# Kernel tuning notes

Hardware: AMD Instinct MI355X
Metric: run time of the kernel (lower is better)

The kernel has to match this reference:

```python
import jax, jax.numpy as jnp
import numpy as np

EMB, GCN = 256, 256
N_REL = 200
B, E, TOPK = 256, 100000, 64
N_PREV, N_ENT, N_TIME = 50000, 20000, 2000


def _linear(x, w, b):
    # torch nn.Linear convention: w is [out, in]
    return x @ w.T + b


def setup_inputs() -> dict:
    key = jax.random.key(0)
    ks = jax.random.split(key, 32)
    nrm = lambda k, s: (jax.random.normal(k, s, jnp.float32) * 0.05)
    # facts columns: b, n, h, r, t, ts. b built so every batch has >= TOPK facts.
    b_col = jax.random.permutation(ks[0], jnp.arange(E, dtype=jnp.int32) % B)
    n_col = jax.random.randint(ks[1], (E,), 0, N_PREV, jnp.int32)
    h_col = jax.random.randint(ks[2], (E,), 0, N_ENT, jnp.int32)
    r_col = jax.random.randint(ks[3], (E,), 0, N_REL, jnp.int32)  # r+1 indexes [zero;rel]
    t_col = jax.random.randint(ks[4], (E,), 0, N_ENT, jnp.int32)
    ts_col = jax.random.randint(ks[5], (E,), 0, N_TIME, jnp.int32)
    facts = jnp.stack([b_col, n_col, h_col, r_col, t_col, ts_col], axis=1)
    return {
        "query_time": jax.random.randint(ks[6], (B,), 0, N_TIME, jnp.int32),  # unused by forward
        "query_emd": nrm(ks[7], (B, EMB)),
        "temp_neighbors_facts": facts,
        "ent_emd": nrm(ks[8], (N_ENT, GCN)),
        "rel_emd": nrm(ks[9], (N_REL, GCN)),
        "hidden_node": nrm(ks[10], (N_PREV, EMB)),
        "hidden_rel": nrm(ks[11], (N_PREV, EMB)),
        "hidden_time": nrm(ks[12], (N_PREV, EMB)),  # unused by forward
        "att_agg": jax.random.uniform(ks[13], (N_PREV,), jnp.float32),
        "time_emd": nrm(ks[14], (N_TIME, EMB)),
        "zero_rel_emd": nrm(ks[15], (1, GCN)),
        "W_message_w": nrm(ks[16], (EMB, 2 * EMB)), "W_message_b": jnp.zeros((EMB,), jnp.float32),
        "att_1_w": nrm(ks[17], (1, 3 * EMB)), "att_1_b": jnp.zeros((1,), jnp.float32),
        "att_2_w": nrm(ks[18], (1, EMB)), "att_2_b": jnp.zeros((1,), jnp.float32),
        "W_h_w": nrm(ks[19], (EMB, 2 * EMB)), "W_h_b": jnp.zeros((EMB,), jnp.float32),
        "lin_e_ts_w": nrm(ks[20], (EMB, GCN + EMB)), "lin_e_ts_b": jnp.zeros((EMB,), jnp.float32),
        "lin_r_ts_w": nrm(ks[21], (EMB, GCN)), "lin_r_ts_b": jnp.zeros((EMB,), jnp.float32),
        "lin_time_w": nrm(ks[22], (EMB, EMB)), "lin_time_b": jnp.zeros((EMB,), jnp.float32),
        "gru_w_ih": nrm(ks[23], (3 * EMB, EMB)), "gru_w_hh": nrm(ks[24], (3 * EMB, EMB)),
        "gru_b_ih": jnp.zeros((3 * EMB,), jnp.float32), "gru_b_hh": jnp.zeros((3 * EMB,), jnp.float32),
        "batch_size": B, "device": 0, "max_nodes": TOPK,
    }


def reference(query_time, query_emd, temp_neighbors_facts, ent_emd, rel_emd,
              hidden_node, hidden_rel, hidden_time, att_agg, time_emd,
              zero_rel_emd, W_message_w, W_message_b, att_1_w, att_1_b,
              att_2_w, att_2_b, W_h_w, W_h_b, lin_e_ts_w, lin_e_ts_b,
              lin_r_ts_w, lin_r_ts_b, lin_time_w, lin_time_b,
              gru_w_ih, gru_w_hh, gru_b_ih, gru_b_hh,
              batch_size, device, max_nodes):
    f = temp_neighbors_facts
    b, n, r, t, ts = f[:, 0], f[:, 1], f[:, 3], f[:, 4], f[:, 5]

    hidden_node_pre = hidden_node[n]            # [E, EMB]
    hidden_rel_pre = hidden_rel[n]              # [E, EMB]
    rel_all = jnp.concatenate([zero_rel_emd, rel_emd], axis=0)
    h_r = rel_all[r + 1]                        # [E, GCN]
    h_ts_raw = time_emd[ts]                     # [E, EMB]
    h_t = _linear(jnp.concatenate([ent_emd[t], h_ts_raw], -1), lin_e_ts_w, lin_e_ts_b)
    h_r = _linear(h_r, lin_r_ts_w, lin_r_ts_b)
    _ = _linear(h_ts_raw, lin_time_w, lin_time_b)  # computed but unused in original

    message = _linear(jnp.concatenate([hidden_node_pre, h_r], -1), W_message_w, W_message_b)
    att_input = jnp.concatenate([query_emd[b], message, h_t], -1)  # [E, 3*EMB]
    att1 = jax.nn.sigmoid(_linear(att_input, att_1_w, att_1_b))[:, 0]

    # single-step GRU (torch nn.GRU gate math)
    gi = h_r @ gru_w_ih.T + gru_b_ih            # [E, 3*EMB]
    gh = hidden_rel_pre @ gru_w_hh.T + gru_b_hh
    i_r, i_z, i_n = jnp.split(gi, 3, axis=-1)
    h_rg, h_zg, h_ng = jnp.split(gh, 3, axis=-1)
    rg = jax.nn.sigmoid(i_r + h_rg)
    zg = jax.nn.sigmoid(i_z + h_zg)
    ng = jnp.tanh(i_n + rg * h_ng)
    hidden_rel_new = (1.0 - zg) * ng + zg * hidden_rel_pre

    att2 = jax.nn.sigmoid(_linear(hidden_rel_new, att_2_w, att_2_b))[:, 0]
    attention = (att1 + att2) * 0.5

    # vectorized per-batch top-k (each batch is guaranteed >= max_nodes facts)
    order = jnp.lexsort((-attention, b))        # sort by batch asc, attention desc
    counts = jax.ops.segment_sum(jnp.ones_like(b), b, num_segments=batch_size)
    starts = jnp.cumsum(counts) - counts
    sel = (starts[:, None] + jnp.arange(max_nodes)[None, :]).reshape(-1)
    new_index = order[sel]                      # [B*topk]

    facts_k = f[new_index]
    message = message[new_index]
    hidden_rel_new = hidden_rel_new[new_index]
    attention = (att1[new_index] + att2[new_index]) * 0.5
    b_k, n_k = facts_k[:, 0], facts_k[:, 1]
    attention = attention * att_agg[n_k]
    M = b_k.shape[0]

    rows = facts_k[:, jnp.array([0, 4, 5])]     # (b, t, ts)
    tail_nodes, tail_index = jnp.unique(rows, axis=0, size=M, fill_value=0, return_inverse=True)
    tail_index = tail_index.reshape(-1)

    tail_emd = _linear(jnp.concatenate([ent_emd[tail_nodes[:, 1]], time_emd[tail_nodes[:, 2]]], -1),
                       lin_e_ts_w, lin_e_ts_b)

    # group_max_norm: normalize attention by per-batch sum (0/0 -> 0)
    den = jax.ops.segment_sum(attention, b_k, num_segments=batch_size)[b_k]
    safe_den = jnp.where(den != 0, den, 1.0)
    attention = jnp.where(den != 0, attention / safe_den, 0.0)

    message_agg = jax.ops.segment_sum(attention[:, None] * message, tail_index, num_segments=M)
    hidden_node_new = _linear(jnp.concatenate([message_agg, tail_emd], -1), W_h_w, W_h_b)  # act = identity
    hidden_rel_out = jax.ops.segment_sum(attention[:, None] * hidden_rel_new, tail_index, num_segments=M)
    att_agg_new = jax.ops.segment_sum(attention, tail_index, num_segments=M)
    return tail_nodes, hidden_node_new, hidden_rel_out, att_agg_new
```

## Files before the change

### kernel.cpp

```cpp
#include <hip/hip_runtime.h>
#include <hip/hip_bf16.h>

#define E_N    100000
#define B_N    256
#define TOPK   64
#define NPREV  50000
#define NENT   20000
#define NTIME  2000
#define NREL   200
#define M_OUT  16384
#define NT8    6250

static __device__ __forceinline__ float sigm(float x){ return 1.f/(1.f+expf(-x)); }

__global__ void zero_kernel(unsigned* __restrict__ p, int n){
  int i = blockIdx.x*256 + threadIdx.x;
  if (i < n) p[i] = 0u;
}

__global__ void pack_w_kernel(const float* __restrict__ w_msg,
                              const float* __restrict__ w_hh,
                              const float* __restrict__ lets_w,
                              const float* __restrict__ w_h,
                              float4* __restrict__ wP,
                              float4* __restrict__ wPL,
                              float4* __restrict__ wPH){
  int i = blockIdx.x*256 + threadIdx.x;
  if (i < 65536){
    int t = i & 255, mat = (i >> 8) & 3, kblk = i >> 10;
    float4 v;
    if (mat == 0) v = *(const float4*)&w_msg[(size_t)t*512 + kblk*4];
    else          v = *(const float4*)&w_hh[(size_t)((mat-1)*256 + t)*256 + kblk*4];
    wP[i] = v;
  } else if (i < 98304){
    int j = i - 65536;
    int t = j & 255, mat = (j >> 8) & 1, kblk = j >> 9;
    wPL[j] = *(const float4*)&lets_w[(size_t)t*512 + mat*256 + kblk*4];
  } else if (i < 131072){
    int j = i - 98304;
    int t = j & 255, kblk = j >> 8;
    wPH[j] = *(const float4*)&w_h[(size_t)t*512 + kblk*4];
  }
}

__global__ void matvec_fused(const float* __restrict__ w_msg,
                             const float* __restrict__ lets_w,
                             const float* __restrict__ lets_b,
                             const float* __restrict__ att1w,
                             const float* __restrict__ att1b,
                             float* __restrict__ wm1a, float* __restrict__ ve,
                             float* __restrict__ vts, float* __restrict__ consts){
  int blk = blockIdx.x, t = threadIdx.x;
  if (blk == 3){
    if (t < 64){
      float p = 0.f;
      for (int d = t; d < 256; d += 64) p += lets_b[d]*att1w[512+d];
      for (int o = 32; o > 0; o >>= 1) p += __shfl_down(p, o);
      if (t == 0) consts[0] = att1b[0] + p;
    }
    return;
  }
  const float* M; int moff; const float* v; float* out;
  if (blk == 0){ M = w_msg;  moff = 0;   v = att1w+256; out = wm1a; }
  else if (blk == 1){ M = lets_w; moff = 0;   v = att1w+512; out = ve; }
  else { M = lets_w; moff = 256; v = att1w+512; out = vts; }
  float acc = 0.f;
  for (int d = 0; d < 256; ++d) acc += M[(size_t)d*512 + moff + t] * v[d];
  out[t] = acc;
}

__global__ void rows_dot_multi(
    const float* __restrict__ A0, const float* __restrict__ v0, float* __restrict__ o0, int n0,
    const float* __restrict__ A1, const float* __restrict__ v1, float* __restrict__ o1_, int n1,
    const float* __restrict__ A2, const float* __restrict__ v2, float* __restrict__ o2, int n2,
    const float* __restrict__ A3, const float* __restrict__ v3, float* __restrict__ o3, int n3,
    const float* __restrict__ A4, const float* __restrict__ v4, float* __restrict__ o4, int n4){
  int gid = blockIdx.x*256 + threadIdx.x;
  int wid = gid >> 6, lane = gid & 63;
  const float* A; const float* v; float* o; int r;
  if (wid < n0){ A=A0; v=v0; o=o0; r=wid; }
  else if ((wid -= n0) < n1){ A=A1; v=v1; o=o1_; r=wid; }
  else if ((wid -= n1) < n2){ A=A2; v=v2; o=o2; r=wid; }
  else if ((wid -= n2) < n3){ A=A3; v=v3; o=o3; r=wid; }
  else if ((wid -= n3) < n4){ A=A4; v=v4; o=o4; r=wid; }
  else return;
  const float* row = A + (size_t)r*256;
  float p = 0.f;
  for (int k = lane; k < 256; k += 64) p += row[k]*v[k];
  for (int off = 32; off > 0; off >>= 1) p += __shfl_down(p, off);
  if (lane == 0) o[r] = p;
}

template<int ND>
__global__ __launch_bounds__(256) void tile_linear(
    const float* __restrict__ A, int lda,
    const float* __restrict__ Bw, int ldb, int boff,
    const float* __restrict__ bias,
    float* __restrict__ out, int ldo, int rows){
  __shared__ float a_s[16][260];
  int tile0 = blockIdx.x*16;
  for (int idx = threadIdx.x; idx < 16*256; idx += 256){
    int i = idx >> 8, k = idx & 255;
    int row = tile0 + i;
    a_s[i][k] = (row < rows) ? A[(size_t)row*lda + k] : 0.f;
  }
  __syncthreads();
  int d = threadIdx.x;
  const float* brow[ND];
  #pragma unroll
  for (int q = 0; q < ND; ++q) brow[q] = Bw + (size_t)(d + 256*q)*ldb + boff;
  float acc[ND][16];
  #pragma unroll
  for (int q = 0; q < ND; ++q){
    float bv = bias ? bias[d + 256*q] : 0.f;
    #pragma unroll
    for (int i = 0; i < 16; ++i) acc[q][i] = bv;
  }
  for (int k = 0; k < 256; k += 4){
    float4 w[ND];
    #pragma unroll
    for (int q = 0; q < ND; ++q) w[q] = *(const float4*)(brow[q] + k);
    #pragma unroll
    for (int i = 0; i < 16; ++i){
      float4 a = *(const float4*)&a_s[i][k];
      #pragma unroll
      for (int q = 0; q < ND; ++q)
        acc[q][i] += w[q].x*a.x + w[q].y*a.y + w[q].z*a.z + w[q].w*a.w;
    }
  }
  #pragma unroll
  for (int i = 0; i < 16; ++i){
    int row = tile0 + i;
    if (row < rows){
      #pragma unroll
      for (int q = 0; q < ND; ++q) out[(size_t)row*ldo + d + 256*q] = acc[q][i];
    }
  }
}

__global__ __launch_bounds__(256) void gemv_ets(
    const float* __restrict__ act, const float4* __restrict__ wPL, int matsel,
    const float* __restrict__ bias, float* __restrict__ out){
  int tile0 = blockIdx.x*16, t = threadIdx.x;
  float acc[16];
  float bv = bias ? bias[t] : 0.f;
  #pragma unroll
  for (int p = 0; p < 16; ++p) acc[p] = bv;
  float4 w = wPL[matsel*256 + t];
  for (int kb = 0; kb < 64; ++kb){
    int kbn = (kb + 1) & 63;
    float4 nw = wPL[(kbn*2 + matsel)*256 + t];
    int k = kb*4;
    #pragma unroll
    for (int p = 0; p < 16; ++p){
      float4 a = *(const float4*)&act[(size_t)(tile0+p)*256 + k];
      acc[p] += w.x*a.x + w.y*a.y + w.z*a.z + w.w*a.w;
    }
    w = nw;
  }
  #pragma unroll
  for (int p = 0; p < 16; ++p)
    out[(size_t)(tile0+p)*256 + t] = acc[p];
}

__global__ void hist2_kernel(const int* __restrict__ facts,
                             int* __restrict__ cnt_t, int* __restrict__ cnt_b){
  int e = blockIdx.x*256 + threadIdx.x;
  if (e < E_N){
    atomicAdd(&cnt_t[facts[e*6+1] >> 3], 1);
    atomicAdd(&cnt_b[facts[e*6+0]], 1);
  }
}

__global__ void scan2_kernel(const int* __restrict__ cnt_t, int* __restrict__ off_t, int* __restrict__ cur_t,
                             const int* __restrict__ cnt_b, int* __restrict__ off_b, int* __restrict__ cur_b){
  const int* cnt; int* off; int* cur; int n;
  if (blockIdx.x == 0){ cnt = cnt_t; off = off_t; cur = cur_t; n = NT8; }
  else { cnt = cnt_b; off = off_b; cur = cur_b; n = B_N; }
  int lane = threadIdx.x;
  int run = 0;
  int npad = (n + 63) & ~63;
  for (int base = 0; base < npad; base += 64){
    int idx = base + lane;
    int orig = (idx < n) ? cnt[idx] : 0;
    int v = orig;
    for (int o = 1; o < 64; o <<= 1){ int t = __shfl_up(v, o); if (lane >= o) v += t; }
    if (idx < n){ int ex = run + v - orig; off[idx] = ex; cur[idx] = ex; }
    run += __shfl(v, 63);
  }
  if (lane == 0) off[n] = E_N;
}

__global__ void scatter2_kernel(const int* __restrict__ facts,
                                int* __restrict__ cur_t, int* __restrict__ edges_t,
                                int* __restrict__ cur_b, int* __restrict__ edges_b){
  int e = blockIdx.x*256 + threadIdx.x;
  if (e < E_N){
    int pt = atomicAdd(&cur_t[facts[e*6+1] >> 3], 1);
    edges_t[pt] = e;
    int pb = atomicAdd(&cur_b[facts[e*6+0]], 1);
    edges_b[pb] = e;
  }
}

__global__ __launch_bounds__(256) void att_kernel(
    const float* __restrict__ hidden_rel,
    const float4* __restrict__ wP,
    const float* __restrict__ b_hh,
    const float* __restrict__ gi,
    const float* __restrict__ att2w, const float* __restrict__ att2b,
    const int* __restrict__ facts,
    const int* __restrict__ bin_off, const int* __restrict__ bin_edges,
    const float* __restrict__ qdot, const float* __restrict__ sn_m,
    const float* __restrict__ sr_m, const float* __restrict__ se,
    const float* __restrict__ st,   const float* __restrict__ consts,
    float* __restrict__ attention){
  __shared__ float gh_s[8][776];
  int tile0 = blockIdx.x*8;
  int t = threadIdx.x;

  float acc[3][8];
  #pragma unroll
  for (int q = 0; q < 3; ++q)
    #pragma unroll
    for (int p = 0; p < 8; ++p) acc[q][p] = 0.f;

  float4 w1 = wP[256 + t], w2 = wP[512 + t], w3 = wP[768 + t];
  for (int kb = 0; kb < 64; ++kb){
    int kbn = (kb + 1) & 63;
    int nb = (kbn*4)*256 + t;
    float4 nw1 = wP[nb + 256], nw2 = wP[nb + 512], nw3 = wP[nb + 768];
    int k = kb*4;
    #pragma unroll
    for (int p = 0; p < 8; ++p){
      float4 a = *(const float4*)&hidden_rel[(size_t)(tile0+p)*256 + k];
      acc[0][p] += w1.x*a.x + w1.y*a.y + w1.z*a.z + w1.w*a.w;
      acc[1][p] += w2.x*a.x + w2.y*a.y + w2.z*a.z + w2.w*a.w;
      acc[2][p] += w3.x*a.x + w3.y*a.y + w3.z*a.z + w3.w*a.w;
    }
    w1 = nw1; w2 = nw2; w3 = nw3;
  }
  #pragma unroll
  for (int q = 0; q < 3; ++q){
    float bv = b_hh[t + 256*q];
    #pragma unroll
    for (int p = 0; p < 8; ++p)
      gh_s[p][t + 256*q] = acc[q][p] + bv;
  }
  __syncthreads();

  int wv = t >> 6, l = t & 63;
  int o0 = bin_off[blockIdx.x], o1 = bin_off[blockIdx.x + 1];
  int d0 = 4*l;
  float4 a2 = *(const float4*)&att2w[d0];
  float c1 = consts[0];
  float a2b = att2b[0];
  for (int idx = o0 + wv; idx < o1; idx += 4){
    int e  = bin_edges[idx];
    int b  = facts[e*6+0], n = facts[e*6+1], r = facts[e*6+3];
    int t_ = facts[e*6+4], ts_ = facts[e*6+5];
    int nl = n - tile0;
    float4 ghr = *(const float4*)&gh_s[nl][d0];
    float4 ghz = *(const float4*)&gh_s[nl][256+d0];
    float4 ghn = *(const float4*)&gh_s[nl][512+d0];
    const float* girow = gi + (size_t)r*768;
    float4 gir = *(const float4*)&girow[d0];
    float4 giz = *(const float4*)&girow[256+d0];
    float4 gin = *(const float4*)&girow[512+d0];
    float4 hp  = *(const float4*)&hidden_rel[(size_t)n*256 + d0];
    float partial;
    {
      float rg = sigm(gir.x + ghr.x), zg = sigm(giz.x + ghz.x);
      float ng = tanhf(gin.x + rg*ghn.x);
      partial = a2.x * ((1.f - zg)*ng + zg*hp.x);
    }{
      float rg = sigm(gir.y + ghr.y), zg = sigm(giz.y + ghz.y);
      float ng = tanhf(gin.y + rg*ghn.y);
      partial += a2.y * ((1.f - zg)*ng + zg*hp.y);
    }{
      float rg = sigm(gir.z + ghr.z), zg = sigm(giz.z + ghz.z);
      float ng = tanhf(gin.z + rg*ghn.z);
      partial += a2.z * ((1.f - zg)*ng + zg*hp.z);
    }{
      float rg = sigm(gir.w + ghr.w), zg = sigm(giz.w + ghz.w);
      float ng = tanhf(gin.w + rg*ghn.w);
      partial += a2.w * ((1.f - zg)*ng + zg*hp.w);
    }
    #pragma unroll
    for (int o = 32; o > 0; o >>= 1) partial += __shfl_xor(partial, o);
    if (l == 0){
      float att2 = sigm(partial + a2b);
      float x1 = qdot[b] + sn_m[n] + sr_m[r] + se[t_] + st[ts_] + c1;
      attention[e] = 0.5f*(sigm(x1) + att2);
    }
  }
}

__global__ __launch_bounds__(256) void topk_kernel(
    const int* __restrict__ facts, const float* __restrict__ attention,
    const float* __restrict__ att_agg,
    const int* __restrict__ boff, const int* __restrict__ bedges,
    int* __restrict__ sel_edge, float* __restrict__ att_norm,
    unsigned* __restrict__ skey, int* __restrict__ Ub){
  __shared__ float sa[512];
  __shared__ int   si[512];
  __shared__ unsigned sk[64];
  int b = blockIdx.x, tid = threadIdx.x;
  sa[tid] = -1.f; sa[tid+256] = -1.f;
  si[tid] = 0x7fffffff; si[tid+256] = 0x7fffffff;
  __syncthreads();
  int o0 = boff[b], cnt = boff[b+1] - o0;
  for (int i = tid; i < cnt; i += 256){
    int e = bedges[o0 + i];
    sa[i] = attention[e]; si[i] = e;
  }
  __syncthreads();
  for (int k = 2; k <= 512; k <<= 1){
    for (int j = k >> 1; j > 0; j >>= 1){
      for (int i0 = tid; i0 < 512; i0 += 256){
        int l = i0 ^ j;
        if (l > i0){
          float ai = sa[i0], al = sa[l];
          int   ii = si[i0], il = si[l];
          bool lFirst = (al > ai) || (al == ai && il < ii);
          bool up = ((i0 & k) == 0);
          if (up ? lFirst : !lFirst){
            sa[i0] = al; sa[l] = ai; si[i0] = il; si[l] = ii;
          }
        }
      }
      __syncthreads();
    }
  }
  if (tid < 64){
    int e = si[tid];
    bool valid = (e != 0x7fffffff);
    if (!valid) e = 0;
    int n = facts[e*6+1];
    float a = valid ? sa[tid]*att_agg[n] : 0.f;
    float den = a;
    for (int o = 32; o > 0; o >>= 1) den += __shfl_down(den, o);
    den = __shfl(den, 0);
    float norm = (den != 0.f) ? a/den : 0.f;
    sel_edge[b*64 + tid] = e;
    att_norm[b*64 + tid] = norm;
    int t_ = facts[e*6+4], ts_ = facts[e*6+5];
    unsigned key = (((unsigned)t_) << 11) | (unsigned)ts_;
    sk[tid] = (key << 6) | (unsigned)tid;
  }
  __syncthreads();
  for (int k = 2; k <= 64; k <<= 1){
    for (int j = k >> 1; j > 0; j >>= 1){
      unsigned nv = 0; bool act = tid < 64;
      if (act){
        unsigned mine = sk[tid], other = sk[tid ^ j];
        bool up = ((tid & k) == 0);
        bool keepmin = (up == ((tid & j) == 0));
        nv = keepmin ? (mine < other ? mine : other) : (mine > other ? mine : other);
      }
      __syncthreads();
      if (act) sk[tid] = nv;
      __syncthreads();
    }
  }
  if (tid < 64){
    unsigned kk = sk[tid];
    skey[b*64 + tid] = kk;
    bool head = (tid == 0) || ((kk >> 6) != (sk[tid-1] >> 6));
    unsigned long long bal = __ballot(head);
    if (tid == 0) Ub[b] = __popcll(bal);
  }
}

__global__ void offs_scan_kernel(const int* __restrict__ Ub, int* __restrict__ offs){
  int lane = threadIdx.x;
  int run = 0;
  for (int base = 0; base < 256; base += 64){
    int orig = Ub[base + lane];
    int v = orig;
    for (int o = 1; o < 64; o <<= 1){ int t = __shfl_up(v, o); if (lane >= o) v += t; }
    offs[base + lane] = run + v - orig;
    run += __shfl(v, 63);
  }
  if (lane == 0) offs[256] = run;
}

__global__ void emit_kernel(const unsigned* __restrict__ skey, const int* __restrict__ offs,
                            int* __restrict__ us, int* __restrict__ tails,
                            float* __restrict__ out_tail){
  int b = blockIdx.x, tid = threadIdx.x;
  unsigned kk = skey[b*64 + tid];
  bool head = (tid == 0) || ((kk >> 6) != (skey[b*64 + tid - 1] >> 6));
  unsigned long long bal = __ballot(head);
  unsigned long long mask_le = (tid == 63) ? ~0ull : ((1ull << (tid+1)) - 1ull);
  int ulocal = __popcll(bal & mask_le) - 1;
  int u = offs[b] + ulocal;
  us[b*64 + tid] = u;
  if (head){
    unsigned key = kk >> 6;
    int t_ = (int)(key >> 11), ts_ = (int)(key & 2047u);
    tails[u*3+0] = b; tails[u*3+1] = t_; tails[u*3+2] = ts_;
    out_tail[u*3+0] = (float)b;
    out_tail[u*3+1] = (float)t_;
    out_tail[u*3+2] = (float)ts_;
  }
}

__global__ __launch_bounds__(256) void sel_kernel(
    const unsigned* __restrict__ skey, const int* __restrict__ sel_edge,
    const float* __restrict__ att_norm, const int* __restrict__ facts,
    const float* __restrict__ hidden_node, const float* __restrict__ hidden_rel,
    const float4* __restrict__ wP,
    const float* __restrict__ msg_r, const float* __restrict__ gi,
    const float* __restrict__ b_hh,
    float* __restrict__ msg_sel, float* __restrict__ hrn_sel){
  __shared__ int n_s[8], r_s[8];
  __shared__ float av_s[8];
  int base = blockIdx.x*8;
  int t = threadIdx.x;
  if (t < 8){
    int gs = base + t;
    int b = gs >> 6, i = gs & 63;
    int j = (int)(skey[(size_t)b*64 + i] & 63u);
    int s = b*64 + j;
    int e = sel_edge[s];
    n_s[t] = facts[e*6+1];
    r_s[t] = facts[e*6+3];
    av_s[t] = att_norm[s];
  }
  __syncthreads();

  float acc[4][8];
  #pragma unroll
  for (int q = 0; q < 4; ++q)
    #pragma unroll
    for (int e = 0; e < 8; ++e) acc[q][e] = 0.f;

  float4 w0 = wP[t], w1 = wP[256 + t], w2 = wP[512 + t], w3 = wP[768 + t];
  for (int kb = 0; kb < 64; ++kb){
    int kbn = (kb + 1) & 63;
    int nb = (kbn*4)*256 + t;
    float4 nw0 = wP[nb], nw1 = wP[nb + 256], nw2 = wP[nb + 512], nw3 = wP[nb + 768];
    int k = kb*4;
    #pragma unroll
    for (int e = 0; e < 8; ++e){
      float4 an = *(const float4*)&hidden_node[(size_t)n_s[e]*256 + k];
      float4 ah = *(const float4*)&hidden_rel[(size_t)n_s[e]*256 + k];
      acc[0][e] += w0.x*an.x + w0.y*an.y + w0.z*an.z + w0.w*an.w;
      acc[1][e] += w1.x*ah.x + w1.y*ah.y + w1.z*ah.z + w1.w*ah.w;
      acc[2][e] += w2.x*ah.x + w2.y*ah.y + w2.z*ah.z + w2.w*ah.w;
      acc[3][e] += w3.x*ah.x + w3.y*ah.y + w3.z*ah.z + w3.w*ah.w;
    }
    w0 = nw0; w1 = nw1; w2 = nw2; w3 = nw3;
  }

  float bhr = b_hh[t], bhz = b_hh[256+t], bhn = b_hh[512+t];
  #pragma unroll
  for (int e = 0; e < 8; ++e){
    int r = r_s[e]; float a = av_s[e];
    const float* girow = gi + (size_t)r*768;
    float msgv = acc[0][e] + msg_r[(size_t)r*256 + t];
    float rg = sigm(girow[t]      + acc[1][e] + bhr);
    float zg = sigm(girow[256+t]  + acc[2][e] + bhz);
    float ng = tanhf(girow[512+t] + rg*(acc[3][e] + bhn));
    float hp = hidden_rel[(size_t)n_s[e]*256 + t];
    float hrn = (1.f - zg)*ng + zg*hp;
    size_t o = (size_t)(base + e)*256 + t;
    msg_sel[o] = a*msgv;
    hrn_sel[o] = a*hrn;
  }
}

__global__ __launch_bounds__(256) void segsum_kernel(
    const unsigned* __restrict__ skey, const int* __restrict__ us,
    const float* __restrict__ att_norm,
    const float* __restrict__ msg_sel, const float* __restrict__ hrn_sel,
    float* __restrict__ msg_agg, float* __restrict__ out_hrel,
    float* __restrict__ out_aagg){
  int b = blockIdx.x, d = threadIdx.x;
  float accm = 0.f, acch = 0.f, acca = 0.f;
  int ucur = -1;
  for (int i = 0; i < 64; ++i){
    int u = us[b*64 + i];
    if (u != ucur){
      if (ucur >= 0){
        msg_agg[(size_t)ucur*256 + d] = accm;
        out_hrel[(size_t)ucur*256 + d] = acch;
        if (d == 0) out_aagg[ucur] = acca;
      }
      ucur = u; accm = 0.f; acch = 0.f; acca = 0.f;
    }
    size_t o = (size_t)(b*64 + i)*256 + d;
    accm += msg_sel[o];
    acch += hrn_sel[o];
    int j = (int)(skey[b*64 + i] & 63u);
    acca += att_norm[b*64 + j];
  }
  if (ucur >= 0){
    msg_agg[(size_t)ucur*256 + d] = accm;
    out_hrel[(size_t)ucur*256 + d] = acch;
    if (d == 0) out_aagg[ucur] = acca;
  }
}

__global__ __launch_bounds__(256) void final_kernel(
    const float* __restrict__ msg_agg, const int* __restrict__ tails,
    const float* __restrict__ ent_t, const float* __restrict__ time_t,
    const float4* __restrict__ wPH,
    const float* __restrict__ b_h,
    float* __restrict__ out_hn){
  int tile0 = blockIdx.x*16, t = threadIdx.x;
  int tu[16], tsu[16];
  #pragma unroll
  for (int p = 0; p < 16; ++p){
    tu[p]  = tails[(tile0+p)*3+1];
    tsu[p] = tails[(tile0+p)*3+2];
  }
  float acc[16];
  float bv = b_h[t];
  #pragma unroll
  for (int p = 0; p < 16; ++p) acc[p] = bv;
  float4 w = wPH[t];
  for (int kb = 0; kb < 128; ++kb){
    int kbn = (kb + 1) & 127;
    float4 nw = wPH[kbn*256 + t];
    if (kb < 64){
      int k = kb*4;
      #pragma unroll
      for (int p = 0; p < 16; ++p){
        float4 a = *(const float4*)&msg_agg[(size_t)(tile0+p)*256 + k];
        acc[p] += w.x*a.x + w.y*a.y + w.z*a.z + w.w*a.w;
      }
    } else {
      int k = (kb-64)*4;
      #pragma unroll
      for (int p = 0; p < 16; ++p){
        float4 a1 = *(const float4*)&ent_t[(size_t)tu[p]*256 + k];
        float4 a2 = *(const float4*)&time_t[(size_t)tsu[p]*256 + k];
        float ax = a1.x + a2.x, ay = a1.y + a2.y, az = a1.z + a2.z, aw = a1.w + a2.w;
        acc[p] += w.x*ax + w.y*ay + w.z*az + w.w*aw;
      }
    }
    w = nw;
  }
  #pragma unroll
  for (int p = 0; p < 16; ++p)
    out_hn[(size_t)(tile0+p)*256 + t] = acc[p];
}

extern "C" void kernel_launch(void* const* d_in, const int* in_sizes, int n_in,
                              void* d_out, int out_size, void* d_ws, size_t ws_size,
                              hipStream_t stream){
  const float* query_emd   = (const float*)d_in[1];
  const int*   facts       = (const int*)  d_in[2];
  const float* ent_emd     = (const float*)d_in[3];
  const float* rel_emd     = (const float*)d_in[4];
  const float* hidden_node = (const float*)d_in[5];
  const float* hidden_rel  = (const float*)d_in[6];
  const float* att_agg     = (const float*)d_in[8];
  const float* time_emd    = (const float*)d_in[9];
  const float* w_msg       = (const float*)d_in[11];
  const float* b_msg       = (const float*)d_in[12];
  const float* att1w       = (const float*)d_in[13];
  const float* att1b       = (const float*)d_in[14];
  const float* att2w       = (const float*)d_in[15];
  const float* att2b       = (const float*)d_in[16];
  const float* w_h         = (const float*)d_in[17];
  const float* b_h         = (const float*)d_in[18];
  const float* lets_w      = (const float*)d_in[19];
  const float* lets_b      = (const float*)d_in[20];
  const float* lrts_w      = (const float*)d_in[21];
  const float* lrts_b      = (const float*)d_in[22];
  const float* w_ih        = (const float*)d_in[25];
  const float* w_hh        = (const float*)d_in[26];
  const float* b_ih        = (const float*)d_in[27];
  const float* b_hh        = (const float*)d_in[28];

  char* p = (char*)d_ws;
  auto alloc = [&](size_t bytes) -> void* {
    void* r = (void*)p; p += (bytes + 255) & ~(size_t)255; return r;
  };
  char* zstart = p;
  int* bin_cnt  = (int*)alloc(6272*4);
  int* bin_cur  = (int*)alloc(6272*4);
  int* bcnt     = (int*)alloc(256*4);
  int* bcur     = (int*)alloc(256*4);
  int* tails    = (int*)alloc((size_t)M_OUT*3*4);
  float* msg_agg= (float*)alloc((size_t)M_OUT*256*4);
  size_t zero_words = (size_t)(p - zstart)/4;
  int* bin_off  = (int*)alloc(6272*4);
  int* bin_edges= (int*)alloc(E_N*4);
  int* boff     = (int*)alloc(257*4);
  int* bedges   = (int*)alloc(E_N*4);
  float* attention = (float*)alloc(E_N*4);
  float* qdot   = (float*)alloc(256*4);
  float* sn_m   = (float*)alloc(NPREV*4);
  float* se     = (float*)alloc(NENT*4);
  float* st     = (float*)alloc(NTIME*4);
  float* sr_m   = (float*)alloc(NREL*4);
  float* wm1a   = (float*)alloc(256*4);
  float* ve     = (float*)alloc(256*4);
  float* vts    = (float*)alloc(256*4);
  float* consts = (float*)alloc(8*4);
  float* hr2    = (float*)alloc((size_t)NREL*256*4);
  float* msg_r  = (float*)alloc((size_t)NREL*256*4);
  float* gi     = (float*)alloc((size_t)NREL*768*4);
  float* time_t = (float*)alloc((size_t)NTIME*256*4);
  float* ent_t  = (float*)alloc((size_t)NENT*256*4);
  float4* wP    = (float4*)alloc((size_t)65536*16);
  float4* wPL   = (float4*)alloc((size_t)32768*16);
  float4* wPH   = (float4*)alloc((size_t)32768*16);
  int* sel_edge = (int*)alloc(M_OUT*4);
  float* att_nrm= (float*)alloc(M_OUT*4);
  unsigned* skey= (unsigned*)alloc(M_OUT*4);
  int* Ub       = (int*)alloc(256*4);
  int* offs     = (int*)alloc(257*4);
  int* us       = (int*)alloc(M_OUT*4);
  float* msg_sel= (float*)alloc((size_t)M_OUT*256*4);
  float* hrn_sel= (float*)alloc((size_t)M_OUT*256*4);
  (void)ws_size; (void)in_sizes; (void)n_in;

  float* out_f     = (float*)d_out;
  float* out_tail  = out_f;
  float* out_hn    = out_f + (size_t)M_OUT*3;
  float* out_hrel  = out_f + (size_t)M_OUT*3 + (size_t)M_OUT*256;
  float* out_aagg  = out_f + (size_t)M_OUT*3 + (size_t)2*M_OUT*256;

  zero_kernel<<<(out_size+255)/256, 256, 0, stream>>>((unsigned*)d_out, out_size);
  zero_kernel<<<((int)zero_words+255)/256, 256, 0, stream>>>((unsigned*)zstart, (int)zero_words);

  pack_w_kernel<<<512, 256, 0, stream>>>(w_msg, w_hh, lets_w, w_h, wP, wPL, wPH);
  matvec_fused<<<4, 256, 0, stream>>>(w_msg, lets_w, lets_b, att1w, att1b, wm1a, ve, vts, consts);

  tile_linear<1><<<(NREL+15)/16, 256, 0, stream>>>(rel_emd, 256, lrts_w, 256, 0, lrts_b, hr2, 256, NREL);
  tile_linear<1><<<(NREL+15)/16, 256, 0, stream>>>(hr2, 256, w_msg, 512, 256, b_msg, msg_r, 256, NREL);
  tile_linear<3><<<(NREL+15)/16, 256, 0, stream>>>(hr2, 256, w_ih, 256, 0, b_ih, gi, 768, NREL);

  gemv_ets<<<NENT/16, 256, 0, stream>>>(ent_emd, wPL, 0, lets_b, ent_t);
  gemv_ets<<<NTIME/16, 256, 0, stream>>>(time_emd, wPL, 1, (const float*)nullptr, time_t);

  {
    int total_rows = B_N + NPREV + NENT + NTIME + NREL;
    int blocks = (total_rows*64 + 255)/256;
    rows_dot_multi<<<blocks, 256, 0, stream>>>(
        query_emd, att1w, qdot, B_N,
        hidden_node, wm1a, sn_m, NPREV,
        ent_emd, ve, se, NENT,
        time_emd, vts, st, NTIME,
        msg_r, att1w+256, sr_m, NREL);
  }

  hist2_kernel<<<(E_N+255)/256, 256, 0, stream>>>(facts, bin_cnt, bcnt);
  scan2_kernel<<<2, 64, 0, stream>>>(bin_cnt, bin_off, bin_cur, bcnt, boff, bcur);
  scatter2_kernel<<<(E_N+255)/256, 256, 0, stream>>>(facts, bin_cur, bin_edges, bcur, bedges);

  att_kernel<<<NT8, 256, 0, stream>>>(hidden_rel, wP, b_hh, gi, att2w, att2b,
      facts, bin_off, bin_edges, qdot, sn_m, sr_m, se, st, consts, attention);

  topk_kernel<<<B_N, 256, 0, stream>>>(facts, attention, att_agg, boff, bedges,
      sel_edge, att_nrm, skey, Ub);
  offs_scan_kernel<<<1, 64, 0, stream>>>(Ub, offs);
  emit_kernel<<<B_N, 64, 0, stream>>>(skey, offs, us, tails, out_tail);
  sel_kernel<<<M_OUT/8, 256, 0, stream>>>(skey, sel_edge, att_nrm, facts,
      hidden_node, hidden_rel, wP, msg_r, gi, b_hh, msg_sel, hrn_sel);
  segsum_kernel<<<B_N, 256, 0, stream>>>(skey, us, att_nrm, msg_sel, hrn_sel,
      msg_agg, out_hrel, out_aagg);
  final_kernel<<<M_OUT/16, 256, 0, stream>>>(msg_agg, tails, ent_t, time_t, wPH, b_h, out_hn);
}
```

Baseline: 1.264 ms.

## Split GRU gh GEMM from edge attention into chunked passes; widen sel tiles

The fused att_kernel, which computed the per-node GRU hidden projection in LDS and then processed that bin's edges, is split into a separate 16-row gemm_gh kernel writing gh to a global scratch buffer and a grid-strided att_edge kernel. This runs in three node chunks so the scratch fits in the msg_sel buffer. The aim is to raise the rows per GEMM tile and balance edge work across blocks, at the cost of extra global traffic for gh. The bin scan becomes a single 256-thread LDS scan, sel_kernel processes 16 edges per block without weight prefetch, and the ent/time projections move later so they can reuse buffer space.

```diff
diff --git a/kernel.cpp b/kernel.cpp
--- a/kernel.cpp
+++ b/kernel.cpp
@@ -10,6 +10,8 @@
 #define NREL   200
 #define M_OUT  16384
 #define NT8    6250
+#define GH_NODES 16672
+#define GH_BINS  2084
 
 static __device__ __forceinline__ float sigm(float x){ return 1.f/(1.f+expf(-x)); }
 
@@ -65,6 +67,7 @@
   else if (blk == 1){ M = lets_w; moff = 0;   v = att1w+512; out = ve; }
   else { M = lets_w; moff = 256; v = att1w+512; out = vts; }
   float acc = 0.f;
+  #pragma unroll 8
   for (int d = 0; d < 256; ++d) acc += M[(size_t)d*512 + moff + t] * v[d];
   out[t] = acc;
 }
@@ -172,23 +175,39 @@
   }
 }
 
-__global__ void scan2_kernel(const int* __restrict__ cnt_t, int* __restrict__ off_t, int* __restrict__ cur_t,
-                             const int* __restrict__ cnt_b, int* __restrict__ off_b, int* __restrict__ cur_b){
-  const int* cnt; int* off; int* cur; int n;
-  if (blockIdx.x == 0){ cnt = cnt_t; off = off_t; cur = cur_t; n = NT8; }
-  else { cnt = cnt_b; off = off_b; cur = cur_b; n = B_N; }
-  int lane = threadIdx.x;
-  int run = 0;
-  int npad = (n + 63) & ~63;
-  for (int base = 0; base < npad; base += 64){
-    int idx = base + lane;
-    int orig = (idx < n) ? cnt[idx] : 0;
-    int v = orig;
-    for (int o = 1; o < 64; o <<= 1){ int t = __shfl_up(v, o); if (lane >= o) v += t; }
-    if (idx < n){ int ex = run + v - orig; off[idx] = ex; cur[idx] = ex; }
-    run += __shfl(v, 63);
-  }
-  if (lane == 0) off[n] = E_N;
+__global__ __launch_bounds__(256) void scan2_lds(
+    const int* __restrict__ cnt_t, int* __restrict__ off_t, int* __restrict__ cur_t,
+    const int* __restrict__ cnt_b, int* __restrict__ off_b, int* __restrict__ cur_b){
+  __shared__ int buf[6272];
+  __shared__ int sums[256];
+  int t = threadIdx.x;
+  int c0 = t*25, c1 = c0 + 25; if (c1 > NT8) c1 = NT8; if (c0 > NT8) c0 = NT8;
+  int s = 0;
+  for (int i = c0; i < c1; ++i){ buf[i] = s; s += cnt_t[i]; }
+  sums[t] = s;
+  __syncthreads();
+  for (int o = 1; o < 256; o <<= 1){
+    int v = (t >= o) ? sums[t-o] : 0;
+    __syncthreads();
+    sums[t] += v;
+    __syncthreads();
+  }
+  int add = (t == 0) ? 0 : sums[t-1];
+  for (int i = c0; i < c1; ++i){ int v = buf[i] + add; off_t[i] = v; cur_t[i] = v; }
+  if (t == 0) off_t[NT8] = E_N;
+  __syncthreads();
+  int orig = cnt_b[t];
+  sums[t] = orig;
+  __syncthreads();
+  for (int o = 1; o < 256; o <<= 1){
+    int v = (t >= o) ? sums[t-o] : 0;
+    __syncthreads();
+    sums[t] += v;
+    __syncthreads();
+  }
+  int ex = sums[t] - orig;
+  off_b[t] = ex; cur_b[t] = ex;
+  if (t == 0) off_b[B_N] = E_N;
 }
 
 __global__ void scatter2_kernel(const int* __restrict__ facts,
@@ -203,27 +222,16 @@
   }
 }
 
-__global__ __launch_bounds__(256) void att_kernel(
-    const float* __restrict__ hidden_rel,
-    const float4* __restrict__ wP,
-    const float* __restrict__ b_hh,
-    const float* __restrict__ gi,
-    const float* __restrict__ att2w, const float* __restrict__ att2b,
-    const int* __restrict__ facts,
-    const int* __restrict__ bin_off, const int* __restrict__ bin_edges,
-    const float* __restrict__ qdot, const float* __restrict__ sn_m,
-    const float* __restrict__ sr_m, const float* __restrict__ se,
-    const float* __restrict__ st,   const float* __restrict__ consts,
-    float* __restrict__ attention){
-  __shared__ float gh_s[8][776];
-  int tile0 = blockIdx.x*8;
+__global__ __launch_bounds__(256) void gemm_gh(
+    const float* __restrict__ hidden_rel, const float4* __restrict__ wP,
+    const float* __restrict__ b_hh, float* __restrict__ gh, int n0){
+  int tile0 = n0 + blockIdx.x*16;
   int t = threadIdx.x;
-
-  float acc[3][8];
+  float acc[3][16];
   #pragma unroll
   for (int q = 0; q < 3; ++q)
     #pragma unroll
-    for (int p = 0; p < 8; ++p) acc[q][p] = 0.f;
+    for (int p = 0; p < 16; ++p) acc[q][p] = 0.f;
 
   float4 w1 = wP[256 + t], w2 = wP[512 + t], w3 = wP[768 + t];
   for (int kb = 0; kb < 64; ++kb){
@@ -232,8 +240,9 @@
     float4 nw1 = wP[nb + 256], nw2 = wP[nb + 512], nw3 = wP[nb + 768];
     int k = kb*4;
     #pragma unroll
-    for (int p = 0; p < 8; ++p){
-      float4 a = *(const float4*)&hidden_rel[(size_t)(tile0+p)*256 + k];
+    for (int p = 0; p < 16; ++p){
+      int row = tile0 + p; if (row > NPREV-1) row = NPREV-1;
+      float4 a = *(const float4*)&hidden_rel[(size_t)row*256 + k];
       acc[0][p] += w1.x*a.x + w1.y*a.y + w1.z*a.z + w1.w*a.w;
       acc[1][p] += w2.x*a.x + w2.y*a.y + w2.z*a.z + w2.w*a.w;
       acc[2][p] += w3.x*a.x + w3.y*a.y + w3.z*a.z + w3.w*a.w;
@@ -244,25 +253,35 @@
   for (int q = 0; q < 3; ++q){
     float bv = b_hh[t + 256*q];
     #pragma unroll
-    for (int p = 0; p < 8; ++p)
-      gh_s[p][t + 256*q] = acc[q][p] + bv;
-  }
-  __syncthreads();
-
-  int wv = t >> 6, l = t & 63;
-  int o0 = bin_off[blockIdx.x], o1 = bin_off[blockIdx.x + 1];
-  int d0 = 4*l;
+    for (int p = 0; p < 16; ++p){
+      int n = tile0 + p;
+      if (n < NPREV) gh[(size_t)(n - n0)*768 + t + 256*q] = acc[q][p] + bv;
+    }
+  }
+}
+
+__global__ __launch_bounds__(256) void att_edge(
+    const float* __restrict__ gh, const float* __restrict__ hidden_rel,
+    const float* __restrict__ gi, const float* __restrict__ att2w,
+    const float* __restrict__ att2b,
+    const int* __restrict__ facts, const int* __restrict__ bin_off,
+    const int* __restrict__ bin_edges,
+    const float* __restrict__ qdot, const float* __restrict__ sn_m,
+    const float* __restrict__ sr_m, const float* __restrict__ se,
+    const float* __restrict__ st, const float* __restrict__ consts,
+    float* __restrict__ attention, int n0, int binLo, int binHi){
+  int t = threadIdx.x, wv = t >> 6, l = t & 63, d0 = 4*l;
+  int idx0 = bin_off[binLo], idx1 = bin_off[binHi];
   float4 a2 = *(const float4*)&att2w[d0];
-  float c1 = consts[0];
-  float a2b = att2b[0];
-  for (int idx = o0 + wv; idx < o1; idx += 4){
+  float c1 = consts[0], a2b = att2b[0];
+  for (int idx = idx0 + blockIdx.x*4 + wv; idx < idx1; idx += 4*2048){
     int e  = bin_edges[idx];
     int b  = facts[e*6+0], n = facts[e*6+1], r = facts[e*6+3];
     int t_ = facts[e*6+4], ts_ = facts[e*6+5];
-    int nl = n - tile0;
-    float4 ghr = *(const float4*)&gh_s[nl][d0];
-    float4 ghz = *(const float4*)&gh_s[nl][256+d0];
-    float4 ghn = *(const float4*)&gh_s[nl][512+d0];
+    const float* ghrow = gh + (size_t)(n - n0)*768;
+    float4 ghr = *(const float4*)&ghrow[d0];
+    float4 ghz = *(const float4*)&ghrow[256+d0];
+    float4 ghn = *(const float4*)&ghrow[512+d0];
     const float* girow = gi + (size_t)r*768;
     float4 gir = *(const float4*)&girow[d0];
     float4 giz = *(const float4*)&girow[256+d0];
@@ -414,11 +433,11 @@
     const float* __restrict__ msg_r, const float* __restrict__ gi,
     const float* __restrict__ b_hh,
     float* __restrict__ msg_sel, float* __restrict__ hrn_sel){
-  __shared__ int n_s[8], r_s[8];
-  __shared__ float av_s[8];
-  int base = blockIdx.x*8;
+  __shared__ int n_s[16], r_s[16];
+  __shared__ float av_s[16];
+  int base = blockIdx.x*16;
   int t = threadIdx.x;
-  if (t < 8){
+  if (t < 16){
     int gs = base + t;
     int b = gs >> 6, i = gs & 63;
     int j = (int)(skey[(size_t)b*64 + i] & 63u);
@@ -430,39 +449,34 @@
   }
   __syncthreads();
 
-  float acc[4][8];
-  #pragma unroll
-  for (int q = 0; q < 4; ++q)
-    #pragma unroll
-    for (int e = 0; e < 8; ++e) acc[q][e] = 0.f;
-
-  float4 w0 = wP[t], w1 = wP[256 + t], w2 = wP[512 + t], w3 = wP[768 + t];
+  float accM[16], accR[16], accZ[16], accN[16];
+  #pragma unroll
+  for (int e = 0; e < 16; ++e){ accM[e]=0.f; accR[e]=0.f; accZ[e]=0.f; accN[e]=0.f; }
+
   for (int kb = 0; kb < 64; ++kb){
-    int kbn = (kb + 1) & 63;
-    int nb = (kbn*4)*256 + t;
-    float4 nw0 = wP[nb], nw1 = wP[nb + 256], nw2 = wP[nb + 512], nw3 = wP[nb + 768];
+    int nb = (kb*4)*256 + t;
+    float4 w0 = wP[nb], w1 = wP[nb + 256], w2 = wP[nb + 512], w3 = wP[nb + 768];
     int k = kb*4;
     #pragma unroll
-    for (int e = 0; e < 8; ++e){
+    for (int e = 0; e < 16; ++e){
       float4 an = *(const float4*)&hidden_node[(size_t)n_s[e]*256 + k];
       float4 ah = *(const float4*)&hidden_rel[(size_t)n_s[e]*256 + k];
-      acc[0][e] += w0.x*an.x + w0.y*an.y + w0.z*an.z + w0.w*an.w;
-      acc[1][e] += w1.x*ah.x + w1.y*ah.y + w1.z*ah.z + w1.w*ah.w;
-      acc[2][e] += w2.x*ah.x + w2.y*ah.y + w2.z*ah.z + w2.w*ah.w;
-      acc[3][e] += w3.x*ah.x + w3.y*ah.y + w3.z*ah.z + w3.w*ah.w;
-    }
-    w0 = nw0; w1 = nw1; w2 = nw2; w3 = nw3;
+      accM[e] += w0.x*an.x + w0.y*an.y + w0.z*an.z + w0.w*an.w;
+      accR[e] += w1.x*ah.x + w1.y*ah.y + w1.z*ah.z + w1.w*ah.w;
+      accZ[e] += w2.x*ah.x + w2.y*ah.y + w2.z*ah.z + w2.w*ah.w;
+      accN[e] += w3.x*ah.x + w3.y*ah.y + w3.z*ah.z + w3.w*ah.w;
+    }
   }
 
   float bhr = b_hh[t], bhz = b_hh[256+t], bhn = b_hh[512+t];
   #pragma unroll
-  for (int e = 0; e < 8; ++e){
+  for (int e = 0; e < 16; ++e){
     int r = r_s[e]; float a = av_s[e];
     const float* girow = gi + (size_t)r*768;
-    float msgv = acc[0][e] + msg_r[(size_t)r*256 + t];
-    float rg = sigm(girow[t]      + acc[1][e] + bhr);
-    float zg = sigm(girow[256+t]  + acc[2][e] + bhz);
-    float ng = tanhf(girow[512+t] + rg*(acc[3][e] + bhn));
+    float msgv = accM[e] + msg_r[(size_t)r*256 + t];
+    float rg = sigm(girow[t]      + accR[e] + bhr);
+    float zg = sigm(girow[256+t]  + accZ[e] + bhz);
+    float ng = tanhf(girow[512+t] + rg*(accN[e] + bhn));
     float hp = hidden_rel[(size_t)n_s[e]*256 + t];
     float hrn = (1.f - zg)*ng + zg*hp;
     size_t o = (size_t)(base + e)*256 + t;
@@ -588,6 +602,11 @@
   int* tails    = (int*)alloc((size_t)M_OUT*3*4);
   float* msg_agg= (float*)alloc((size_t)M_OUT*256*4);
   size_t zero_words = (size_t)(p - zstart)/4;
+  float* msg_sel= (float*)alloc((size_t)M_OUT*256*4);
+  float* hrn_sel= (float*)alloc((size_t)M_OUT*256*4);
+  float* ent_t  = (float*)alloc((size_t)NENT*256*4);
+  float* time_t = (float*)alloc((size_t)NTIME*256*4);
+  float* gh     = msg_sel;
   int* bin_off  = (int*)alloc(6272*4);
   int* bin_edges= (int*)alloc(E_N*4);
   int* boff     = (int*)alloc(257*4);
@@ -605,8 +624,6 @@
   float* hr2    = (float*)alloc((size_t)NREL*256*4);
   float* msg_r  = (float*)alloc((size_t)NREL*256*4);
   float* gi     = (float*)alloc((size_t)NREL*768*4);
-  float* time_t = (float*)alloc((size_t)NTIME*256*4);
-  float* ent_t  = (float*)alloc((size_t)NENT*256*4);
   float4* wP    = (float4*)alloc((size_t)65536*16);
   float4* wPL   = (float4*)alloc((size_t)32768*16);
   float4* wPH   = (float4*)alloc((size_t)32768*16);
@@ -616,8 +633,6 @@
   int* Ub       = (int*)alloc(256*4);
   int* offs     = (int*)alloc(257*4);
   int* us       = (int*)alloc(M_OUT*4);
-  float* msg_sel= (float*)alloc((size_t)M_OUT*256*4);
-  float* hrn_sel= (float*)alloc((size_t)M_OUT*256*4);
   (void)ws_size; (void)in_sizes; (void)n_in;
 
   float* out_f     = (float*)d_out;
@@ -635,9 +650,6 @@
   tile_linear<1><<<(NREL+15)/16, 256, 0, stream>>>(rel_emd, 256, lrts_w, 256, 0, lrts_b, hr2, 256, NREL);
   tile_linear<1><<<(NREL+15)/16, 256, 0, stream>>>(hr2, 256, w_msg, 512, 256, b_msg, msg_r, 256, NREL);
   tile_linear<3><<<(NREL+15)/16, 256, 0, stream>>>(hr2, 256, w_ih, 256, 0, b_ih, gi, 768, NREL);
-
-  gemv_ets<<<NENT/16, 256, 0, stream>>>(ent_emd, wPL, 0, lets_b, ent_t);
-  gemv_ets<<<NTIME/16, 256, 0, stream>>>(time_emd, wPL, 1, (const float*)nullptr, time_t);
 
   {
     int total_rows = B_N + NPREV + NENT + NTIME + NREL;
@@ -651,17 +663,28 @@
   }
 
   hist2_kernel<<<(E_N+255)/256, 256, 0, stream>>>(facts, bin_cnt, bcnt);
-  scan2_kernel<<<2, 64, 0, stream>>>(bin_cnt, bin_off, bin_cur, bcnt, boff, bcur);
+  scan2_lds<<<1, 256, 0, stream>>>(bin_cnt, bin_off, bin_cur, bcnt, boff, bcur);
   scatter2_kernel<<<(E_N+255)/256, 256, 0, stream>>>(facts, bin_cur, bin_edges, bcur, bedges);
 
-  att_kernel<<<NT8, 256, 0, stream>>>(hidden_rel, wP, b_hh, gi, att2w, att2b,
-      facts, bin_off, bin_edges, qdot, sn_m, sr_m, se, st, consts, attention);
+  for (int pass = 0; pass < 3; ++pass){
+    int n0 = pass*GH_NODES;
+    int binLo = pass*GH_BINS;
+    int binHi = (pass == 2) ? NT8 : (binLo + GH_BINS);
+    gemm_gh<<<GH_NODES/16, 256, 0, stream>>>(hidden_rel, wP, b_hh, gh, n0);
+    att_edge<<<2048, 256, 0, stream>>>(gh, hidden_rel, gi, att2w, att2b,
+        facts, bin_off, bin_edges, qdot, sn_m, sr_m, se, st, consts,
+        attention, n0, binLo, binHi);
+  }
 
   topk_kernel<<<B_N, 256, 0, stream>>>(facts, attention, att_agg, boff, bedges,
       sel_edge, att_nrm, skey, Ub);
   offs_scan_kernel<<<1, 64, 0, stream>>>(Ub, offs);
   emit_kernel<<<B_N, 64, 0, stream>>>(skey, offs, us, tails, out_tail);
-  sel_kernel<<<M_OUT/8, 256, 0, stream>>>(skey, sel_edge, att_nrm, facts,
+
+  gemv_ets<<<NENT/16, 256, 0, stream>>>(ent_emd, wPL, 0, lets_b, ent_t);
+  gemv_ets<<<NTIME/16, 256, 0, stream>>>(time_emd, wPL, 1, (const float*)nullptr, time_t);
+
+  sel_kernel<<<M_OUT/16, 256, 0, stream>>>(skey, sel_edge, att_nrm, facts,
       hidden_node, hidden_rel, wP, msg_r, gi, b_hh, msg_sel, hrn_sel);
   segsum_kernel<<<B_N, 256, 0, stream>>>(skey, us, att_nrm, msg_sel, hrn_sel,
       msg_agg, out_hrel, out_aagg);
```

Result: slower. 1.547 ms (+22.4%).
